# Kernel tuning notes

Hardware: AMD Instinct MI355X
Metric: run time of the kernel (lower is better)

## Reference

```python
import jax, jax.numpy as jnp
import numpy as np

NUM_NODES = 6144
INPUT_DIM = 128
OUTPUT_DIM = 128
NUM_HEADS = 4
HEAD_DIM = OUTPUT_DIM // NUM_HEADS
NEG_INF = -9e15  # mask constant used by the original module


def setup_inputs() -> dict:
    key = jax.random.key(0)
    k_x, k_adj, k_W, k_a = jax.random.split(key, 4)
    x = jax.random.normal(k_x, (NUM_NODES, INPUT_DIM), dtype=jnp.float32)
    adj = jax.random.randint(k_adj, (NUM_NODES, NUM_NODES), 0, 2, dtype=jnp.int32)
    # kaiming-uniform-ish init scale
    W = jax.random.uniform(k_W, (NUM_HEADS, INPUT_DIM, HEAD_DIM), dtype=jnp.float32,
                           minval=-1.0, maxval=1.0) * np.sqrt(6.0 / INPUT_DIM)
    a = jax.random.uniform(k_a, (NUM_HEADS, 2 * HEAD_DIM, 1), dtype=jnp.float32,
                           minval=-1.0, maxval=1.0) * np.sqrt(6.0 / (2 * HEAD_DIM))
    return {"x": x, "adj": adj, "W": W, "a": a}


def reference(x, adj, W, a):
    # x: [N, Din], adj: [N, N] int, W: [H, Din, d], a: [H, 2d, 1]
    H, Din, d = W.shape
    N = x.shape[0]
    h = jnp.einsum('ni,hid->hnd', x, W)               # [H, N, d] per-head projections
    a_dst = a[:, :d, 0]                                # applied to h_j (column / source of message)
    a_src = a[:, d:, 0]                                # applied to h_i (row / destination)
    s_dst = jnp.einsum('hnd,hd->hn', h, a_dst)         # [H, N]
    s_src = jnp.einsum('hnd,hd->hn', h, a_src)         # [H, N]
    # energy[h, i, j] = leaky_relu(a1 . h_j + a2 . h_i), same as concat-attention
    energy = jax.nn.leaky_relu(s_src[:, :, None] + s_dst[:, None, :], negative_slope=0.2)
    energy = jnp.where(adj[None] > 0, energy, NEG_INF)  # [H, N, N]
    attention = jax.nn.softmax(energy, axis=-1)
    h_prime = jnp.einsum('hij,hjd->hid', attention, h)  # [H, N, d]
    # faithful to torch h_prime.view(num_nodes, -1) on a contiguous [H,N,d] tensor
    return jnp.reshape(h_prime, (N, H * d))
```

## Files before the change

### kernel.cpp

```cpp
#include <hip/hip_runtime.h>
#include <stdint.h>

#define N_NODES 6144
#define LOG2E 1.44269504088896f

typedef float f32x4 __attribute__((ext_vector_type(4)));
typedef float f32x2 __attribute__((ext_vector_type(2)));
typedef short short8 __attribute__((ext_vector_type(8)));
typedef unsigned int uint32;
typedef unsigned long long uint64;

extern "C" __device__ float __ocml_native_exp2_f32(float);

__device__ __forceinline__ unsigned int pack2bf(float a, float b) {
  unsigned int ua = __float_as_uint(a) + 0x8000u;
  unsigned int ub = __float_as_uint(b) + 0x8000u;
  return __builtin_amdgcn_perm(ub, ua, 0x07060302u);
}

__device__ __forceinline__ uint32 bitmask32(uint32 bits, int j) {
#if __has_builtin(__builtin_amdgcn_sbfe)
  return (uint32)__builtin_amdgcn_sbfe((int)bits, (uint32)j, 1u);
#else
  return (uint32)(((int)(bits << (31 - j))) >> 31);
#endif
}

__global__ __launch_bounds__(256) void k1_feat(const float* __restrict__ x,
                                               const float* __restrict__ W,
                                               const float* __restrict__ a,
                                               unsigned short* __restrict__ hfF,
                                               float* __restrict__ s_src2,
                                               float* __restrict__ s_dst2) {
  __shared__ float xl[64][132];
  __shared__ float Wl[64][128];
  int t = threadIdx.x;
  int n0 = blockIdx.x * 64;
  for (int u = t; u < 2048; u += 256) {
    int row = u >> 5, c4 = (u & 31) << 2;
    *(float4*)&xl[row][c4] = *(const float4*)(x + (size_t)(n0 + row) * 128 + c4);
  }
  int cg = t & 31, c0 = cg << 2;
  int ng = t >> 5, nb = ng << 3;
  float acc[8][4] = {};
  for (int ic = 0; ic < 2; ++ic) {
    __syncthreads();
    for (int u = t; u < 2048; u += 256) {
      int ii = u >> 5, c4 = (u & 31) << 2;
      int hh = c4 >> 5, d0 = c4 & 31;
      *(float4*)&Wl[ii][c4] = *(const float4*)(W + hh * 4096 + (ic * 64 + ii) * 32 + d0);
    }
    __syncthreads();
    #pragma unroll 4
    for (int ii = 0; ii < 64; ++ii) {
      float4 wv = *(float4*)&Wl[ii][c0];
      int i = ic * 64 + ii;
      #pragma unroll
      for (int r = 0; r < 8; ++r) {
        float xv = xl[nb + r][i];
        acc[r][0] += xv * wv.x; acc[r][1] += xv * wv.y;
        acc[r][2] += xv * wv.z; acc[r][3] += xv * wv.w;
      }
    }
  }
  __syncthreads();
  unsigned short* tb = (unsigned short*)&xl[0][0];
  float* pb = &Wl[0][0];
  int hh = c0 >> 5, d0 = c0 & 31;
  float4 adv = *(const float4*)(a + hh * 64 + d0);
  float4 asv = *(const float4*)(a + hh * 64 + 32 + d0);
  #pragma unroll
  for (int cc = 0; cc < 4; ++cc) {
    unsigned int* dst = (unsigned int*)(tb + (c0 + cc) * 66 + nb);
    #pragma unroll
    for (int p = 0; p < 4; ++p)
      dst[p] = pack2bf(acc[2 * p][cc], acc[2 * p + 1][cc]);
  }
  #pragma unroll
  for (int r = 0; r < 8; ++r) {
    float pd = acc[r][0] * adv.x + acc[r][1] * adv.y + acc[r][2] * adv.z + acc[r][3] * adv.w;
    float ps = acc[r][0] * asv.x + acc[r][1] * asv.y + acc[r][2] * asv.z + acc[r][3] * asv.w;
    pb[(nb + r) * 33 + cg] = pd;
    pb[2112 + (nb + r) * 33 + cg] = ps;
  }
  __syncthreads();
  {
    #pragma unroll
    for (int p = 0; p < 4; ++p) {
      int chunk = (p << 2) + (t >> 6);
      int lane = t & 63, mm = lane & 15, qq = lane >> 4;
      int h2 = chunk >> 2, kbl = (chunk >> 1) & 1, ff = chunk & 1;
      const unsigned int* s32 = (const unsigned int*)(
          tb + (h2 * 32 + ff * 16 + mm) * 66 + kbl * 32 + (qq << 3));
      int4 v;
      v.x = s32[0]; v.y = s32[1]; v.z = s32[2]; v.w = s32[3];
      int kbg = (n0 >> 5) + kbl;
      *(int4*)(hfF + (size_t)(((h2 * 192 + kbg) * 2 + ff) * 64 + lane) * 8) = v;
    }
  }
  for (int task = t; task < 512; task += 256) {
    int n = task & 63, hz = task >> 6;
    int h = hz & 3, sdx = hz >> 2;
    const float* src = pb + sdx * 2112 + n * 33 + h * 8;
    float s = src[0] + src[1] + src[2] + src[3] + src[4] + src[5] + src[6] + src[7];
    float* out = sdx ? s_src2 : s_dst2;
    out[h * N_NODES + n0 + n] = s * LOG2E;
  }
}

__device__ __forceinline__ void gat_tile(float ss, uint32 bits8,
                                         const f32x2 (&dv)[4], short8 b0, short8 b1,
                                         short8 ones, f32x4& a0, f32x4& a1, f32x4& az) {
  union { uint32 u4[4]; short8 v; } afr;
  f32x2 ss2;
  ss2[0] = ss; ss2[1] = ss;
  #pragma unroll
  for (int p = 0; p < 4; ++p) {
    f32x2 e = ss2 + dv[p];
    f32x2 e5 = e * 0.2f;
    float lrl = fmaxf(e[0], e5[0]);
    float lrh = fmaxf(e[1], e5[1]);
    float exl = __ocml_native_exp2_f32(lrl);
    float exh = __ocml_native_exp2_f32(lrh);
    uint32 wl = __float_as_uint(exl) & bitmask32(bits8, 2 * p);
    uint32 wh = __float_as_uint(exh) & bitmask32(bits8, 2 * p + 1);
    uint32 pk;
    asm("v_cvt_pk_bf16_f32 %0, %1, %2"
        : "=v"(pk)
        : "v"(__uint_as_float(wl)), "v"(__uint_as_float(wh)));
    afr.u4[p] = pk;
  }
  a0 = __builtin_amdgcn_mfma_f32_16x16x32_bf16(afr.v, b0, a0, 0, 0, 0);
  a1 = __builtin_amdgcn_mfma_f32_16x16x32_bf16(afr.v, b1, a1, 0, 0, 0);
  az = __builtin_amdgcn_mfma_f32_16x16x32_bf16(afr.v, ones, az, 0, 0, 0);
}

__device__ __forceinline__ void step2(uint32 w0, uint32 w1,
                                      int sh, const float* sdp, int koff,
                                      int4 B0i, int4 B1i, short8 ones,
                                      float ss0, float ss1,
                                      f32x4& a00, f32x4& a01, f32x4& a10, f32x4& a11,
                                      f32x4& az0, f32x4& az1) {
  union { f32x4 q[2]; f32x2 d[4]; } du;
  du.q[0] = *(const f32x4*)(sdp + koff);
  du.q[1] = *(const f32x4*)(sdp + koff + 4);
  union { int4 i; short8 v; } b0u, b1u;
  b0u.i = B0i; b1u.i = B1i;
  gat_tile(ss0, (w0 >> sh), du.d, b0u.v, b1u.v, ones, a00, a01, az0);
  gat_tile(ss1, (w1 >> sh), du.d, b0u.v, b1u.v, ones, a10, a11, az1);
}

__global__ __launch_bounds__(256, 3) void k2_attn(const int* __restrict__ adj,
                                                  const unsigned short* __restrict__ hfF,
                                                  const float* __restrict__ s_src2,
                                                  const float* __restrict__ s_dst2,
                                                  float* __restrict__ Zpart,
                                                  float* __restrict__ part) {
  __shared__ float sd[4][1536];
  __shared__ uint32 mlds[2][32][4];
  int t = threadIdx.x;
  int h = t >> 6, lane = t & 63, m = lane & 15, quad = lane >> 4;
  int sh = quad << 3;
  int bx = blockIdx.x;
  int slice = bx & 3, mg = bx >> 2;
  int i0 = mg << 5, kbase = slice * 1536;
  {
    const float4* g = (const float4*)s_dst2;
    float4* l = (float4*)sd;
    int kb4 = slice * 384;
    #pragma unroll
    for (int r = 0; r < 6; ++r) {
      int u = t + (r << 8);
      int hx = u / 384, uu = u - hx * 384;
      l[hx * 384 + uu] = g[hx * 1536 + kb4 + uu];
    }
  }
  const int* arow = adj + (size_t)(i0 + (h << 3)) * N_NODES + kbase + lane;
  {
    #pragma unroll
    for (int r = 0; r < 16; ++r) {
      int v = arow[(r >> 1) * N_NODES + ((r & 1) << 6)];
      uint64 b = __ballot(v != 0);
      if (lane == r)
        *(uint64*)&mlds[0][(h << 3) + (r >> 1)][(r & 1) << 1] = b;
    }
  }
  float ss0 = s_src2[h * N_NODES + i0 + m];
  float ss1 = s_src2[h * N_NODES + i0 + 16 + m];
  __syncthreads();

  const unsigned short* hfb = hfF + (size_t)(h * 192 + slice * 48) * 1024 + lane * 8;
  const float* sdp = &sd[h][0] + sh;

  f32x4 a00 = {0,0,0,0}, a01 = {0,0,0,0};
  f32x4 a10 = {0,0,0,0}, a11 = {0,0,0,0};
  f32x4 az0 = {0,0,0,0}, az1 = {0,0,0,0};
  union { uint32 u[4]; short8 v; } ones;
  #pragma unroll
  for (int q = 0; q < 4; ++q) ones.u[q] = 0x3F803F80u;

  #pragma unroll 1
  for (int o = 0; o < 12; ++o) {
    int cur = o & 1, nxt = cur ^ 1;
    const unsigned short* gb = hfb + o * 4096;
    int4 B00 = *(const int4*)(gb);
    int4 B01 = *(const int4*)(gb + 512);
    int4 B10 = *(const int4*)(gb + 1024);
    int4 B11 = *(const int4*)(gb + 1536);
    int4 B20 = *(const int4*)(gb + 2048);
    int4 B21 = *(const int4*)(gb + 2560);
    int4 B30 = *(const int4*)(gb + 3072);
    int4 B31 = *(const int4*)(gb + 3584);
    int pv[16];
    if (o < 11) {
      const int* ap = arow + ((o + 1) << 7);
      #pragma unroll
      for (int r = 0; r < 16; ++r)
        pv[r] = ap[(r >> 1) * N_NODES + ((r & 1) << 6)];
    }
    uint4 M0 = *(const uint4*)&mlds[cur][m][0];
    uint4 M1 = *(const uint4*)&mlds[cur][16 + m][0];
    __builtin_amdgcn_sched_barrier(0);
    int ko = o << 7;
    step2(M0.x, M1.x, sh, sdp, ko,      B00, B01, ones.v, ss0, ss1,
          a00, a01, a10, a11, az0, az1);
    step2(M0.y, M1.y, sh, sdp, ko + 32, B10, B11, ones.v, ss0, ss1,
          a00, a01, a10, a11, az0, az1);
    step2(M0.z, M1.z, sh, sdp, ko + 64, B20, B21, ones.v, ss0, ss1,
          a00, a01, a10, a11, az0, az1);
    step2(M0.w, M1.w, sh, sdp, ko + 96, B30, B31, ones.v, ss0, ss1,
          a00, a01, a10, a11, az0, az1);
    __builtin_amdgcn_sched_barrier(0);
    if (o < 11) {
      #pragma unroll
      for (int r = 0; r < 16; ++r) {
        uint64 b = __ballot(pv[r] != 0);
        if (lane == r)
          *(uint64*)&mlds[nxt][(h << 3) + (r >> 1)][(r & 1) << 1] = b;
      }
    }
    __syncthreads();
  }

  if (m == 0) {
    float* zb = Zpart + (size_t)slice * 24576 + h * N_NODES + i0 + (quad << 2);
    #pragma unroll
    for (int r = 0; r < 4; ++r) {
      zb[r] = az0[r];
      zb[16 + r] = az1[r];
    }
  }
  float* pb = part + (size_t)slice * 786432 + (size_t)h * (N_NODES * 32) +
              (size_t)i0 * 32;
  #pragma unroll
  for (int r = 0; r < 4; ++r) {
    int row = (quad << 2) + r;
    pb[row * 32 + m] = a00[r];
    pb[row * 32 + 16 + m] = a01[r];
    pb[(16 + row) * 32 + m] = a10[r];
    pb[(16 + row) * 32 + 16 + m] = a11[r];
  }
}

__global__ __launch_bounds__(256) void k3_final(const float* __restrict__ part,
                                                const float* __restrict__ Zpart,
                                                float* __restrict__ out) {
  unsigned int idx4 = blockIdx.x * 256 + threadIdx.x;
  unsigned int h = idx4 / 49152u;
  unsigned int i = (idx4 - h * 49152u) >> 3;
  float z = 0.f;
  #pragma unroll
  for (int s = 0; s < 4; ++s) z += Zpart[s * 24576u + h * N_NODES + i];
  f32x4 p = {0.f, 0.f, 0.f, 0.f};
  const f32x4* P = (const f32x4*)part;
  #pragma unroll
  for (int s = 0; s < 4; ++s) p += P[(size_t)s * 196608u + idx4];
  float rz = 1.0f / z;
  ((f32x4*)out)[idx4] = p * rz;
}

extern "C" void kernel_launch(void* const* d_in, const int* in_sizes, int n_in,
                              void* d_out, int out_size, void* d_ws, size_t ws_size,
                              hipStream_t stream) {
  const float* x = (const float*)d_in[0];
  const int* adj = (const int*)d_in[1];
  const float* W = (const float*)d_in[2];
  const float* a = (const float*)d_in[3];
  float* out = (float*)d_out;

  float* wsf = (float*)d_ws;
  unsigned short* hfF = (unsigned short*)wsf;
  float* s_src2 = wsf + 393216;
  float* s_dst2 = s_src2 + 24576;
  float* part   = s_dst2 + 24576;
  float* Zpart  = part + 4 * 786432;

  hipLaunchKernelGGL(k1_feat, dim3(96), dim3(256), 0, stream, x, W, a, hfF, s_src2, s_dst2);
  hipLaunchKernelGGL(k2_attn, dim3(768), dim3(256), 0, stream,
                     adj, hfF, s_src2, s_dst2, Zpart, part);
  hipLaunchKernelGGL(k3_final, dim3(768), dim3(256), 0, stream, part, Zpart, out);
}
```

Baseline: 255.1 us.

## Split feature projection into 8-node blocks and hoist adjacency prologue loads

The projection kernel now runs 768 blocks of 8 nodes instead of 96 blocks of 64. Each thread computes one node and four output columns, reads W directly from global memory (where it should stay cached), and uses warp shuffles to reduce the attention scores. The aim is to fill the device, since 96 blocks left most compute units idle. In the attention kernel, the 16 adjacency loads are issued into registers before the s_dst staging so their latency overlaps that copy, with the ballots done afterwards. The cost is more repeated W reads and more registers held in the prologue.

Result: faster. 247.7 us (-2.9%).

```diff
diff --git a/kernel.cpp b/kernel.cpp
--- a/kernel.cpp
+++ b/kernel.cpp
@@ -11,12 +11,6 @@
 typedef unsigned long long uint64;
 
 extern "C" __device__ float __ocml_native_exp2_f32(float);
-
-__device__ __forceinline__ unsigned int pack2bf(float a, float b) {
-  unsigned int ua = __float_as_uint(a) + 0x8000u;
-  unsigned int ub = __float_as_uint(b) + 0x8000u;
-  return __builtin_amdgcn_perm(ub, ua, 0x07060302u);
-}
 
 __device__ __forceinline__ uint32 bitmask32(uint32 bits, int j) {
 #if __has_builtin(__builtin_amdgcn_sbfe)
@@ -32,79 +26,50 @@
                                                unsigned short* __restrict__ hfF,
                                                float* __restrict__ s_src2,
                                                float* __restrict__ s_dst2) {
-  __shared__ float xl[64][132];
-  __shared__ float Wl[64][128];
+  __shared__ float xA[8][132];
+  __shared__ unsigned short tbp[128][12];
   int t = threadIdx.x;
-  int n0 = blockIdx.x * 64;
-  for (int u = t; u < 2048; u += 256) {
-    int row = u >> 5, c4 = (u & 31) << 2;
-    *(float4*)&xl[row][c4] = *(const float4*)(x + (size_t)(n0 + row) * 128 + c4);
-  }
-  int cg = t & 31, c0 = cg << 2;
-  int ng = t >> 5, nb = ng << 3;
-  float acc[8][4] = {};
-  for (int ic = 0; ic < 2; ++ic) {
-    __syncthreads();
-    for (int u = t; u < 2048; u += 256) {
-      int ii = u >> 5, c4 = (u & 31) << 2;
-      int hh = c4 >> 5, d0 = c4 & 31;
-      *(float4*)&Wl[ii][c4] = *(const float4*)(W + hh * 4096 + (ic * 64 + ii) * 32 + d0);
-    }
-    __syncthreads();
-    #pragma unroll 4
-    for (int ii = 0; ii < 64; ++ii) {
-      float4 wv = *(float4*)&Wl[ii][c0];
-      int i = ic * 64 + ii;
-      #pragma unroll
-      for (int r = 0; r < 8; ++r) {
-        float xv = xl[nb + r][i];
-        acc[r][0] += xv * wv.x; acc[r][1] += xv * wv.y;
-        acc[r][2] += xv * wv.z; acc[r][3] += xv * wv.w;
-      }
-    }
+  int bx = blockIdx.x;
+  int n0 = bx << 3;
+  {
+    int row = t >> 5, c4 = (t & 31) << 2;
+    *(float4*)&xA[row][c4] = *(const float4*)(x + (size_t)(n0 + row) * 128 + c4);
   }
   __syncthreads();
-  unsigned short* tb = (unsigned short*)&xl[0][0];
-  float* pb = &Wl[0][0];
-  int hh = c0 >> 5, d0 = c0 & 31;
+  int r = t & 7, cgA = t >> 3;
+  int hh = cgA >> 3, d0 = (cgA & 7) << 2;
+  const float* wp = W + hh * 4096 + d0;
+  float ac0 = 0.f, ac1 = 0.f, ac2 = 0.f, ac3 = 0.f;
+  #pragma unroll 8
+  for (int i = 0; i < 128; ++i) {
+    float xv = xA[r][i];
+    float4 wv = *(const float4*)(wp + (i << 5));
+    ac0 += xv * wv.x; ac1 += xv * wv.y;
+    ac2 += xv * wv.z; ac3 += xv * wv.w;
+  }
+  int c0 = cgA << 2;
+  tbp[c0 + 0][r] = (unsigned short)((__float_as_uint(ac0) + 0x8000u) >> 16);
+  tbp[c0 + 1][r] = (unsigned short)((__float_as_uint(ac1) + 0x8000u) >> 16);
+  tbp[c0 + 2][r] = (unsigned short)((__float_as_uint(ac2) + 0x8000u) >> 16);
+  tbp[c0 + 3][r] = (unsigned short)((__float_as_uint(ac3) + 0x8000u) >> 16);
   float4 adv = *(const float4*)(a + hh * 64 + d0);
   float4 asv = *(const float4*)(a + hh * 64 + 32 + d0);
-  #pragma unroll
-  for (int cc = 0; cc < 4; ++cc) {
-    unsigned int* dst = (unsigned int*)(tb + (c0 + cc) * 66 + nb);
-    #pragma unroll
-    for (int p = 0; p < 4; ++p)
-      dst[p] = pack2bf(acc[2 * p][cc], acc[2 * p + 1][cc]);
-  }
-  #pragma unroll
-  for (int r = 0; r < 8; ++r) {
-    float pd = acc[r][0] * adv.x + acc[r][1] * adv.y + acc[r][2] * adv.z + acc[r][3] * adv.w;
-    float ps = acc[r][0] * asv.x + acc[r][1] * asv.y + acc[r][2] * asv.z + acc[r][3] * asv.w;
-    pb[(nb + r) * 33 + cg] = pd;
-    pb[2112 + (nb + r) * 33 + cg] = ps;
+  float pd = ac0 * adv.x + ac1 * adv.y + ac2 * adv.z + ac3 * adv.w;
+  float ps = ac0 * asv.x + ac1 * asv.y + ac2 * asv.z + ac3 * asv.w;
+  pd += __shfl_xor(pd, 8); pd += __shfl_xor(pd, 16); pd += __shfl_xor(pd, 32);
+  ps += __shfl_xor(ps, 8); ps += __shfl_xor(ps, 16); ps += __shfl_xor(ps, 32);
+  if (((t & 63) >> 3) == 0) {
+    s_dst2[hh * N_NODES + n0 + r] = pd * LOG2E;
+    s_src2[hh * N_NODES + n0 + r] = ps * LOG2E;
   }
   __syncthreads();
-  {
-    #pragma unroll
-    for (int p = 0; p < 4; ++p) {
-      int chunk = (p << 2) + (t >> 6);
-      int lane = t & 63, mm = lane & 15, qq = lane >> 4;
-      int h2 = chunk >> 2, kbl = (chunk >> 1) & 1, ff = chunk & 1;
-      const unsigned int* s32 = (const unsigned int*)(
-          tb + (h2 * 32 + ff * 16 + mm) * 66 + kbl * 32 + (qq << 3));
-      int4 v;
-      v.x = s32[0]; v.y = s32[1]; v.z = s32[2]; v.w = s32[3];
-      int kbg = (n0 >> 5) + kbl;
-      *(int4*)(hfF + (size_t)(((h2 * 192 + kbg) * 2 + ff) * 64 + lane) * 8) = v;
-    }
-  }
-  for (int task = t; task < 512; task += 256) {
-    int n = task & 63, hz = task >> 6;
-    int h = hz & 3, sdx = hz >> 2;
-    const float* src = pb + sdx * 2112 + n * 33 + h * 8;
-    float s = src[0] + src[1] + src[2] + src[3] + src[4] + src[5] + src[6] + src[7];
-    float* out = sdx ? s_src2 : s_dst2;
-    out[h * N_NODES + n0 + n] = s * LOG2E;
+  if (t < 128) {
+    int h2 = t >> 5, ff = (t >> 4) & 1, mm = t & 15;
+    const uint32* s32 = (const uint32*)&tbp[t][0];
+    int4 v;
+    v.x = s32[0]; v.y = s32[1]; v.z = s32[2]; v.w = s32[3];
+    int kb = bx >> 2, qq = bx & 3;
+    *(int4*)(hfF + (size_t)(((h2 * 192 + kb) * 2 + ff) * 64 + qq * 16 + mm) * 8) = v;
   }
 }
 
@@ -164,6 +129,13 @@
   int bx = blockIdx.x;
   int slice = bx & 3, mg = bx >> 2;
   int i0 = mg << 5, kbase = slice * 1536;
+
+  const int* arow = adj + (size_t)(i0 + (h << 3)) * N_NODES + kbase + lane;
+  int av[16];
+  #pragma unroll
+  for (int r = 0; r < 16; ++r)
+    av[r] = arow[(r >> 1) * N_NODES + ((r & 1) << 6)];
+
   {
     const float4* g = (const float4*)s_dst2;
     float4* l = (float4*)sd;
@@ -175,18 +147,14 @@
       l[hx * 384 + uu] = g[hx * 1536 + kb4 + uu];
     }
   }
-  const int* arow = adj + (size_t)(i0 + (h << 3)) * N_NODES + kbase + lane;
-  {
-    #pragma unroll
-    for (int r = 0; r < 16; ++r) {
-      int v = arow[(r >> 1) * N_NODES + ((r & 1) << 6)];
-      uint64 b = __ballot(v != 0);
-      if (lane == r)
-        *(uint64*)&mlds[0][(h << 3) + (r >> 1)][(r & 1) << 1] = b;
-    }
-  }
   float ss0 = s_src2[h * N_NODES + i0 + m];
   float ss1 = s_src2[h * N_NODES + i0 + 16 + m];
+  #pragma unroll
+  for (int r = 0; r < 16; ++r) {
+    uint64 b = __ballot(av[r] != 0);
+    if (lane == r)
+      *(uint64*)&mlds[0][(h << 3) + (r >> 1)][(r & 1) << 1] = b;
+  }
   __syncthreads();
 
   const unsigned short* hfb = hfF + (size_t)(h * 192 + slice * 48) * 1024 + lane * 8;
@@ -295,7 +263,7 @@
   float* part   = s_dst2 + 24576;
   float* Zpart  = part + 4 * 786432;
 
-  hipLaunchKernelGGL(k1_feat, dim3(96), dim3(256), 0, stream, x, W, a, hfF, s_src2, s_dst2);
+  hipLaunchKernelGGL(k1_feat, dim3(768), dim3(256), 0, stream, x, W, a, hfF, s_src2, s_dst2);
   hipLaunchKernelGGL(k2_attn, dim3(768), dim3(256), 0, stream,
                      adj, hfF, s_src2, s_dst2, Zpart, part);
   hipLaunchKernelGGL(k3_final, dim3(768), dim3(256), 0, stream, part, Zpart, out);
```
